# Kernel tuning notes

Hardware: AMD Instinct MI355X
Metric: run time of the kernel (lower is better)

Reference implementation:

```python
import jax, jax.numpy as jnp
import numpy as np


def setup_inputs() -> dict:
    key = jax.random.key(0)
    ks = jax.random.split(key, 5)
    B, C, H, W = 4, 64, 64, 64
    C8 = C // 8
    return {
        "x_opt": jax.random.normal(ks[0], (B, C, H, W), jnp.float32),
        "x_sar": jax.random.normal(ks[1], (B, C, H, W), jnp.float32),
        "wq": jax.random.normal(ks[2], (C8, C), jnp.float32) * 0.05,
        "bq": jnp.zeros((C8,), jnp.float32),
        "wk": jax.random.normal(ks[3], (C8, C), jnp.float32) * 0.05,
        "bk": jnp.zeros((C8,), jnp.float32),
        "wv": jax.random.normal(ks[4], (C, C), jnp.float32) * 0.05,
        "bv": jnp.zeros((C,), jnp.float32),
        "gamma": jnp.zeros((1,), jnp.float32),
    }


def reference(x_opt, x_sar, wq, bq, wk, bk, wv, bv, gamma):
    b, c, h, w = x_opt.shape
    n = h * w
    xo = x_opt.reshape(b, c, n)  # [b, c, N]
    xs = x_sar.reshape(b, c, n)
    # 1x1 convs == channel matmuls
    q = jnp.einsum('oc,bcn->bon', wq, xo) + bq[None, :, None]  # [b, c//8, N]
    k = jnp.einsum('oc,bcn->bon', wk, xs) + bk[None, :, None]  # [b, c//8, N]
    v = jnp.einsum('oc,bcn->bon', wv, xs) + bv[None, :, None]  # [b, c, N]
    # attn[b, n, m] = softmax_m( q[:, :, n] . k[:, :, m] )  -- NO 1/sqrt(d) scaling
    scores = jnp.einsum('bdn,bdm->bnm', q, k)  # [b, N, N]
    attn = jax.nn.softmax(scores, axis=-1)
    # out[b, c, n] = sum_m v[b, c, m] * attn[b, n, m]
    out = jnp.einsum('bcm,bnm->bcn', v, attn).reshape(b, c, h, w)
    return gamma[0] * out + x_opt
```

## Files before the change

### kernel.cpp

```cpp
#include <hip/hip_runtime.h>
#include <hip/hip_bf16.h>
#include <stdint.h>

#define NDIM 4096
#define CDIM 64
#define NSPLIT 8
#define SPAN (NDIM / NSPLIT)
#define KBLK 128
#define NIT (SPAN / KBLK)
#define LOG2E 1.44269504088896f

typedef float f32x16 __attribute__((ext_vector_type(16)));
typedef short bf16x8 __attribute__((ext_vector_type(8)));
union U4B { uint4 u; bf16x8 b; };

static __device__ __forceinline__ uint32_t cvtpk(float lo, float hi) {
  uint32_t r;
  asm("v_cvt_pk_bf16_f32 %0, %1, %2" : "=v"(r) : "v"(lo), "v"(hi));
  return r;
}
static __device__ __forceinline__ uint16_t f2bf(float f) {
  uint32_t r;
  asm("v_cvt_pk_bf16_f32 %0, %1, %1" : "=v"(r) : "v"(f));
  return (uint16_t)r;
}
static __device__ __forceinline__ float fexp2(float x) {
  return __builtin_amdgcn_exp2f(x);
}
static __device__ __forceinline__ void gload_lds16(const void* g, void* l) {
  __builtin_amdgcn_global_load_lds(
      (const __attribute__((address_space(1))) uint32_t*)g,
      (__attribute__((address_space(3))) uint32_t*)l, 16, 0, 0);
}

__global__ __launch_bounds__(256) void proj_kernel(
    const float* __restrict__ x_opt, const float* __restrict__ x_sar,
    const float* __restrict__ wq, const float* __restrict__ bq,
    const float* __restrict__ wk, const float* __restrict__ bk,
    const float* __restrict__ wvp, const float* __restrict__ bv,
    uint16_t* __restrict__ qf, uint16_t* __restrict__ kf,
    uint16_t* __restrict__ vf)
{
  const int tid = threadIdx.x;
  const int w = tid >> 6;
  const int l = tid & 63;
  const int x = l & 31;
  const int hi = l >> 5;
  const int cg = w >> 1;
  const int half = w & 1;

  const int id = blockIdx.x;
  const int b = id >> 6;
  const int n0 = (id & 63) * 64 + cg * 32;
  const size_t xbase = (size_t)b * CDIM * NDIM;

  bf16x8 xsB[4];
#pragma unroll
  for (int kc = 0; kc < 4; kc++) {
    float sv[8];
#pragma unroll
    for (int j = 0; j < 8; j++)
      sv[j] = x_sar[xbase + (size_t)(kc * 16 + hi * 8 + j) * NDIM + n0 + x];
    U4B us;
    us.u = make_uint4(cvtpk(sv[0], sv[1]), cvtpk(sv[2], sv[3]),
                      cvtpk(sv[4], sv[5]), cvtpk(sv[6], sv[7]));
    xsB[kc] = us.b;
  }

  bf16x8 vA[4];
#pragma unroll
  for (int kc = 0; kc < 4; kc++) {
    const float* wr = wvp + (half * 32 + x) * 64 + kc * 16 + hi * 8;
    float4 wa = ((const float4*)wr)[0];
    float4 wb = ((const float4*)wr)[1];
    U4B u;
    u.u = make_uint4(cvtpk(wa.x, wa.y), cvtpk(wa.z, wa.w),
                     cvtpk(wb.x, wb.y), cvtpk(wb.z, wb.w));
    vA[kc] = u.b;
  }

  const f32x16 z16 = {0.f,0.f,0.f,0.f, 0.f,0.f,0.f,0.f,
                      0.f,0.f,0.f,0.f, 0.f,0.f,0.f,0.f};
  f32x16 aV = z16;
#pragma unroll
  for (int kc = 0; kc < 4; kc++)
    aV = __builtin_amdgcn_mfma_f32_32x32x16_bf16(vA[kc], xsB[kc], aV, 0, 0, 0);
#pragma unroll
  for (int r = 0; r < 16; r++) {
    const int row = half * 32 + (r & 3) + 8 * (r >> 2) + 4 * hi;
    vf[(size_t)(b * 64 + row) * NDIM + n0 + x] = f2bf(aV[r] + bv[row]);
  }

  bf16x8 gA[4], gB[4];
#pragma unroll
  for (int kc = 0; kc < 4; kc++) {
    U4B ua;
    ua.u = make_uint4(0u, 0u, 0u, 0u);
    if (x < 8) {
      const float* wr = (half ? wk : wq) + x * 64 + kc * 16 + hi * 8;
      float4 wa = ((const float4*)wr)[0];
      float4 wb = ((const float4*)wr)[1];
      ua.u = make_uint4(cvtpk(wa.x, wa.y), cvtpk(wa.z, wa.w),
                        cvtpk(wb.x, wb.y), cvtpk(wb.z, wb.w));
    }
    gA[kc] = ua.b;
    if (half == 0) {
      float ov[8];
#pragma unroll
      for (int j = 0; j < 8; j++)
        ov[j] = x_opt[xbase + (size_t)(kc * 16 + hi * 8 + j) * NDIM + n0 + x];
      U4B uo;
      uo.u = make_uint4(cvtpk(ov[0], ov[1]), cvtpk(ov[2], ov[3]),
                        cvtpk(ov[4], ov[5]), cvtpk(ov[6], ov[7]));
      gB[kc] = uo.b;
    } else {
      gB[kc] = xsB[kc];
    }
  }
  f32x16 aG = z16;
#pragma unroll
  for (int kc = 0; kc < 4; kc++)
    aG = __builtin_amdgcn_mfma_f32_32x32x16_bf16(gA[kc], gB[kc], aG, 0, 0, 0);

  const float* bias = half ? bk : bq;
  const float scl = half ? 1.0f : LOG2E;
  float gv[4];
#pragma unroll
  for (int r = 0; r < 4; r++) gv[r] = (aG[r] + bias[4 * hi + r]) * scl;
  uint16_t* dst = half ? kf : qf;
  const size_t nrow = ((size_t)b * NDIM + n0 + x) * 16;
  uint2 st;
  st.x = cvtpk(gv[0], gv[1]); st.y = cvtpk(gv[2], gv[3]);
  *(uint2*)(dst + nrow + hi * 4) = st;
  if (hi == 0) {
    const uint4 z4 = make_uint4(0u, 0u, 0u, 0u);
    *(uint4*)(dst + nrow + 8) = z4;
  }
}

__global__ __launch_bounds__(256, 3) void attn_kernel(
    const uint16_t* __restrict__ qf, const uint16_t* __restrict__ kf,
    const uint16_t* __restrict__ vf,
    uint16_t* __restrict__ po, float* __restrict__ ls)
{
  __shared__ __align__(16) uint16_t vt[2][64][128];

  const int tid = threadIdx.x;
  const int w = tid >> 6;
  const int l = tid & 63;
  const int x = l & 31;
  const int hi = l >> 5;

  const int id = blockIdx.x;
  const int sp = id & 7;
  const int qb = (id >> 3) & 31;
  const int b = id >> 8;

  const int n0 = qb * 128;
  const uint16_t* vsrc = vf + (size_t)b * CDIM * NDIM + sp * SPAN;
  const uint16_t* ksrc = kf + ((size_t)b * NDIM + sp * SPAN) * 16;
  const int qrow = n0 + w * 32 + x;

  U4B qfr;
  qfr.u = *(const uint4*)(qf + ((size_t)b * NDIM + qrow) * 16 + hi * 8);

  const uint32_t xh4 = (uint32_t)(((x & 15) ^ hi) << 4);
  const uint8_t* vbase0 = (const uint8_t*)&vt[0][0][0] + (size_t)x * 256 + xh4;
  const uint8_t* vbase1 = vbase0 + 16384;

  const f32x16 z16 = {0.f,0.f,0.f,0.f, 0.f,0.f,0.f,0.f,
                      0.f,0.f,0.f,0.f, 0.f,0.f,0.f,0.f};
  f32x16 oacc0 = z16, oacc1 = z16;
  float lacc[4] = {0.f, 0.f, 0.f, 0.f};

  auto stageV = [&](int t, int buf) {
#pragma unroll
    for (int si = 0; si < 4; si++) {
      const int rowbase = w * 16 + si * 4;
      const int row = rowbase + (l >> 4);
      gload_lds16(vsrc + (size_t)row * NDIM + t * KBLK +
                      (((l & 15) ^ (row & 15)) << 3),
                  &vt[buf][rowbase][0]);
    }
  };

  stageV(0, 0);
  uint4 kc = *(const uint4*)(ksrc + (size_t)x * 16 + hi * 8);
  __syncthreads();
  uint4 kn = *(const uint4*)(ksrc + ((size_t)32 + x) * 16 + hi * 8);
  U4B ka; ka.u = kc;
  f32x16 scur = __builtin_amdgcn_mfma_f32_32x32x16_bf16(ka.b, qfr.b, z16, 0, 0, 0);
  kc = kn;

#pragma unroll
  for (int gq = 0; gq < 16; gq++) {
    const int it = gq >> 2;
    const int q4 = gq & 3;

    if (q4 == 0 && it + 1 < NIT) stageV(it + 1, (it + 1) & 1);

    uint4 kn2 = *(const uint4*)(ksrc + ((size_t)(gq + 2) * 32 + x) * 16 + hi * 8);

    U4B kb; kb.u = kc;
    f32x16 snxt = __builtin_amdgcn_mfma_f32_32x32x16_bf16(kb.b, qfr.b, z16, 0, 0, 0);
    kc = kn2;

    float p[16];
#pragma unroll
    for (int i = 0; i < 16; i++) p[i] = fexp2(scur[i]);
    float t8[8];
#pragma unroll
    for (int i = 0; i < 8; i++) t8[i] = p[i] + p[i + 8];
#pragma unroll
    for (int i = 0; i < 4; i++) lacc[i] += t8[i] + t8[i + 4];

    uint32_t W[8];
#pragma unroll
    for (int j = 0; j < 8; j++) W[j] = cvtpk(p[2 * j], p[2 * j + 1]);

    const uint8_t* vb = (it & 1) ? vbase1 : vbase0;
    __builtin_amdgcn_s_setprio(1);
#pragma unroll
    for (int sub = 0; sub < 2; sub++) {
      uint32_t a0 = W[sub * 4 + 0], b0 = W[sub * 4 + 2];
      uint32_t a1 = W[sub * 4 + 1], b1 = W[sub * 4 + 3];
      asm("v_permlane32_swap_b32 %0, %1" : "+v"(a0), "+v"(b0));
      asm("v_permlane32_swap_b32 %0, %1" : "+v"(a1), "+v"(b1));
      U4B pf;
      pf.u = make_uint4(a0, a1, b0, b1);
      const uint32_t kb4 = (uint32_t)((q4 * 4 + sub * 2) << 4);
      const uint8_t* va = vb + (kb4 ^ xh4) - xh4;
      U4B vf0, vf1;
      vf0.u = *(const uint4*)(va);
      vf1.u = *(const uint4*)(va + 8192);
      oacc0 = __builtin_amdgcn_mfma_f32_32x32x16_bf16(vf0.b, pf.b, oacc0, 0, 0, 0);
      oacc1 = __builtin_amdgcn_mfma_f32_32x32x16_bf16(vf1.b, pf.b, oacc1, 0, 0, 0);
    }
    __builtin_amdgcn_s_setprio(0);

    if (q4 == 3) __syncthreads();
    scur = snxt;
  }

  uint16_t* prow = po + (((size_t)sp * 4 + b) * NDIM + qrow) * CDIM;
#pragma unroll
  for (int cb = 0; cb < 2; cb++) {
    const f32x16 oa = (cb == 0) ? oacc0 : oacc1;
#pragma unroll
    for (int u = 0; u < 4; u++) {
      uint2 st;
      st.x = cvtpk(oa[u * 4 + 0], oa[u * 4 + 1]);
      st.y = cvtpk(oa[u * 4 + 2], oa[u * 4 + 3]);
      *(uint2*)(prow + cb * 32 + u * 8 + hi * 4) = st;
    }
  }
  float ltot = (lacc[0] + lacc[1]) + (lacc[2] + lacc[3]);
  ltot += __shfl_xor(ltot, 32);
  if (hi == 0)
    ls[((size_t)sp * 4 + b) * NDIM + qrow] = ltot;
}

__global__ __launch_bounds__(256) void merge_kernel(
    const uint16_t* __restrict__ po, const float* __restrict__ ls,
    const float* __restrict__ x_opt, const float* __restrict__ gamma,
    float* __restrict__ out)
{
  __shared__ float ot[32][65];
  const int tid = threadIdx.x;
  const int b = blockIdx.x >> 7;
  const int n0 = (blockIdx.x & 127) * 32;
  {
    const int q = tid >> 3;
    const int co = (tid & 7) * 8;
    const int nq = n0 + q;
    float wsum = 0.f;
    float acc[8] = {0.f, 0.f, 0.f, 0.f, 0.f, 0.f, 0.f, 0.f};
#pragma unroll
    for (int s = 0; s < NSPLIT; s++) {
      wsum += ls[((size_t)s * 4 + b) * NDIM + nq];
      const uint4 pv = *(const uint4*)(po + (((size_t)s * 4 + b) * NDIM + nq) * CDIM + co);
      const uint32_t* pw = (const uint32_t*)&pv;
#pragma unroll
      for (int j = 0; j < 4; j++) {
        acc[j * 2 + 0] += __uint_as_float(pw[j] << 16);
        acc[j * 2 + 1] += __uint_as_float(pw[j] & 0xFFFF0000u);
      }
    }
    const float inv = 1.f / wsum;
#pragma unroll
    for (int j = 0; j < 8; j++) ot[q][co + j] = acc[j] * inv;
  }
  __syncthreads();
  {
    const float gm = gamma[0];
    const int c = tid >> 2;
    const int j8 = (tid & 3) * 8;
    const float* xp = x_opt + ((size_t)b * CDIM + c) * NDIM + n0 + j8;
    float* op = out + ((size_t)b * CDIM + c) * NDIM + n0 + j8;
#pragma unroll
    for (int h = 0; h < 2; h++) {
      float4 xv = ((const float4*)xp)[h];
      float4 ov;
      ov.x = gm * ot[j8 + h * 4 + 0][c] + xv.x;
      ov.y = gm * ot[j8 + h * 4 + 1][c] + xv.y;
      ov.z = gm * ot[j8 + h * 4 + 2][c] + xv.z;
      ov.w = gm * ot[j8 + h * 4 + 3][c] + xv.w;
      ((float4*)op)[h] = ov;
    }
  }
}

extern "C" void kernel_launch(void* const* d_in, const int* in_sizes, int n_in,
                              void* d_out, int out_size, void* d_ws, size_t ws_size,
                              hipStream_t stream) {
  const float* x_opt = (const float*)d_in[0];
  const float* x_sar = (const float*)d_in[1];
  const float* wq    = (const float*)d_in[2];
  const float* bq    = (const float*)d_in[3];
  const float* wk    = (const float*)d_in[4];
  const float* bk    = (const float*)d_in[5];
  const float* wvp   = (const float*)d_in[6];
  const float* bv    = (const float*)d_in[7];
  const float* gamma = (const float*)d_in[8];
  float* outp = (float*)d_out;

  uint16_t* qf = (uint16_t*)d_ws;
  uint16_t* kf = (uint16_t*)((char*)d_ws + 524288);
  uint16_t* vf = (uint16_t*)((char*)d_ws + 1048576);
  uint16_t* po = (uint16_t*)((char*)d_ws + 3145728);
  float* lsp   = (float*)((char*)d_ws + 19922944);

  proj_kernel<<<256, 256, 0, stream>>>(x_opt, x_sar, wq, bq, wk, bk, wvp, bv,
                                       qf, kf, vf);
  attn_kernel<<<1024, 256, 0, stream>>>(qf, kf, vf, po, lsp);
  merge_kernel<<<512, 256, 0, stream>>>(po, lsp, x_opt, gamma, outp);
}
```

Baseline: 38.21 us.

## Split projection work across waves and drop score software-pipelining to raise occupancy

The projection kernel now gives each wave one MFMA chain over a 32-column tile: two waves compute V, one Q, one K. The grid doubles to 512 blocks and each wave does a single 4-MFMA sequence instead of two serial ones, which shortens per-wave latency. In the attention kernel, the one-step-ahead score MFMA prefetch is removed and launch_bounds goes from 3 to 4 waves per SIMD, cutting register pressure so more blocks can be resident. This trades explicit MFMA/exp overlap within a wave for more latency hiding across waves, and the x_sar tile is now loaded by three waves in the same block instead of being reused from registers.

```diff
diff --git a/kernel.cpp b/kernel.cpp
--- a/kernel.cpp
+++ b/kernel.cpp
@@ -46,99 +46,79 @@
   const int l = tid & 63;
   const int x = l & 31;
   const int hi = l >> 5;
-  const int cg = w >> 1;
-  const int half = w & 1;
 
   const int id = blockIdx.x;
-  const int b = id >> 6;
-  const int n0 = (id & 63) * 64 + cg * 32;
+  const int b = id >> 7;
+  const int n0 = (id & 127) * 32;
   const size_t xbase = (size_t)b * CDIM * NDIM;
 
-  bf16x8 xsB[4];
+  const float* xsrc = (w == 2) ? x_opt : x_sar;
+  bf16x8 xB[4];
 #pragma unroll
   for (int kc = 0; kc < 4; kc++) {
     float sv[8];
 #pragma unroll
     for (int j = 0; j < 8; j++)
-      sv[j] = x_sar[xbase + (size_t)(kc * 16 + hi * 8 + j) * NDIM + n0 + x];
+      sv[j] = xsrc[xbase + (size_t)(kc * 16 + hi * 8 + j) * NDIM + n0 + x];
     U4B us;
     us.u = make_uint4(cvtpk(sv[0], sv[1]), cvtpk(sv[2], sv[3]),
                       cvtpk(sv[4], sv[5]), cvtpk(sv[6], sv[7]));
-    xsB[kc] = us.b;
-  }
-
-  bf16x8 vA[4];
-#pragma unroll
-  for (int kc = 0; kc < 4; kc++) {
-    const float* wr = wvp + (half * 32 + x) * 64 + kc * 16 + hi * 8;
-    float4 wa = ((const float4*)wr)[0];
-    float4 wb = ((const float4*)wr)[1];
-    U4B u;
-    u.u = make_uint4(cvtpk(wa.x, wa.y), cvtpk(wa.z, wa.w),
-                     cvtpk(wb.x, wb.y), cvtpk(wb.z, wb.w));
-    vA[kc] = u.b;
-  }
-
-  const f32x16 z16 = {0.f,0.f,0.f,0.f, 0.f,0.f,0.f,0.f,
-                      0.f,0.f,0.f,0.f, 0.f,0.f,0.f,0.f};
-  f32x16 aV = z16;
-#pragma unroll
-  for (int kc = 0; kc < 4; kc++)
-    aV = __builtin_amdgcn_mfma_f32_32x32x16_bf16(vA[kc], xsB[kc], aV, 0, 0, 0);
-#pragma unroll
-  for (int r = 0; r < 16; r++) {
-    const int row = half * 32 + (r & 3) + 8 * (r >> 2) + 4 * hi;
-    vf[(size_t)(b * 64 + row) * NDIM + n0 + x] = f2bf(aV[r] + bv[row]);
-  }
-
-  bf16x8 gA[4], gB[4];
+    xB[kc] = us.b;
+  }
+
+  bf16x8 aF[4];
 #pragma unroll
   for (int kc = 0; kc < 4; kc++) {
     U4B ua;
     ua.u = make_uint4(0u, 0u, 0u, 0u);
-    if (x < 8) {
-      const float* wr = (half ? wk : wq) + x * 64 + kc * 16 + hi * 8;
+    if (w < 2) {
+      const float* wr = wvp + (w * 32 + x) * 64 + kc * 16 + hi * 8;
       float4 wa = ((const float4*)wr)[0];
       float4 wb = ((const float4*)wr)[1];
       ua.u = make_uint4(cvtpk(wa.x, wa.y), cvtpk(wa.z, wa.w),
                         cvtpk(wb.x, wb.y), cvtpk(wb.z, wb.w));
-    }
-    gA[kc] = ua.b;
-    if (half == 0) {
-      float ov[8];
-#pragma unroll
-      for (int j = 0; j < 8; j++)
-        ov[j] = x_opt[xbase + (size_t)(kc * 16 + hi * 8 + j) * NDIM + n0 + x];
-      U4B uo;
-      uo.u = make_uint4(cvtpk(ov[0], ov[1]), cvtpk(ov[2], ov[3]),
-                        cvtpk(ov[4], ov[5]), cvtpk(ov[6], ov[7]));
-      gB[kc] = uo.b;
-    } else {
-      gB[kc] = xsB[kc];
-    }
-  }
-  f32x16 aG = z16;
+    } else if (x < 8) {
+      const float* wr = ((w == 2) ? wq : wk) + x * 64 + kc * 16 + hi * 8;
+      float4 wa = ((const float4*)wr)[0];
+      float4 wb = ((const float4*)wr)[1];
+      ua.u = make_uint4(cvtpk(wa.x, wa.y), cvtpk(wa.z, wa.w),
+                        cvtpk(wb.x, wb.y), cvtpk(wb.z, wb.w));
+    }
+    aF[kc] = ua.b;
+  }
+
+  const f32x16 z16 = {0.f,0.f,0.f,0.f, 0.f,0.f,0.f,0.f,
+                      0.f,0.f,0.f,0.f, 0.f,0.f,0.f,0.f};
+  f32x16 acc = z16;
 #pragma unroll
   for (int kc = 0; kc < 4; kc++)
-    aG = __builtin_amdgcn_mfma_f32_32x32x16_bf16(gA[kc], gB[kc], aG, 0, 0, 0);
-
-  const float* bias = half ? bk : bq;
-  const float scl = half ? 1.0f : LOG2E;
-  float gv[4];
-#pragma unroll
-  for (int r = 0; r < 4; r++) gv[r] = (aG[r] + bias[4 * hi + r]) * scl;
-  uint16_t* dst = half ? kf : qf;
-  const size_t nrow = ((size_t)b * NDIM + n0 + x) * 16;
-  uint2 st;
-  st.x = cvtpk(gv[0], gv[1]); st.y = cvtpk(gv[2], gv[3]);
-  *(uint2*)(dst + nrow + hi * 4) = st;
-  if (hi == 0) {
-    const uint4 z4 = make_uint4(0u, 0u, 0u, 0u);
-    *(uint4*)(dst + nrow + 8) = z4;
-  }
-}
-
-__global__ __launch_bounds__(256, 3) void attn_kernel(
+    acc = __builtin_amdgcn_mfma_f32_32x32x16_bf16(aF[kc], xB[kc], acc, 0, 0, 0);
+
+  if (w < 2) {
+#pragma unroll
+    for (int r = 0; r < 16; r++) {
+      const int row = w * 32 + (r & 3) + 8 * (r >> 2) + 4 * hi;
+      vf[(size_t)(b * 64 + row) * NDIM + n0 + x] = f2bf(acc[r] + bv[row]);
+    }
+  } else {
+    const float* bias = (w == 2) ? bq : bk;
+    const float scl = (w == 2) ? LOG2E : 1.0f;
+    float gv[4];
+#pragma unroll
+    for (int r = 0; r < 4; r++) gv[r] = (acc[r] + bias[4 * hi + r]) * scl;
+    uint16_t* dst = (w == 2) ? qf : kf;
+    const size_t nrow = ((size_t)b * NDIM + n0 + x) * 16;
+    uint2 st;
+    st.x = cvtpk(gv[0], gv[1]); st.y = cvtpk(gv[2], gv[3]);
+    *(uint2*)(dst + nrow + hi * 4) = st;
+    if (hi == 0) {
+      const uint4 z4 = make_uint4(0u, 0u, 0u, 0u);
+      *(uint4*)(dst + nrow + 8) = z4;
+    }
+  }
+}
+
+__global__ __launch_bounds__(256, 4) void attn_kernel(
     const uint16_t* __restrict__ qf, const uint16_t* __restrict__ kf,
     const uint16_t* __restrict__ vf,
     uint16_t* __restrict__ po, float* __restrict__ ls)
@@ -165,7 +145,7 @@
   qfr.u = *(const uint4*)(qf + ((size_t)b * NDIM + qrow) * 16 + hi * 8);
 
   const uint32_t xh4 = (uint32_t)(((x & 15) ^ hi) << 4);
-  const uint8_t* vbase0 = (const uint8_t*)&vt[0][0][0] + (size_t)x * 256 + xh4;
+  const uint8_t* vbase0 = (const uint8_t*)&vt[0][0][0] + (size_t)x * 256;
   const uint8_t* vbase1 = vbase0 + 16384;
 
   const f32x16 z16 = {0.f,0.f,0.f,0.f, 0.f,0.f,0.f,0.f,
@@ -187,10 +167,6 @@
   stageV(0, 0);
   uint4 kc = *(const uint4*)(ksrc + (size_t)x * 16 + hi * 8);
   __syncthreads();
-  uint4 kn = *(const uint4*)(ksrc + ((size_t)32 + x) * 16 + hi * 8);
-  U4B ka; ka.u = kc;
-  f32x16 scur = __builtin_amdgcn_mfma_f32_32x32x16_bf16(ka.b, qfr.b, z16, 0, 0, 0);
-  kc = kn;
 
 #pragma unroll
   for (int gq = 0; gq < 16; gq++) {
@@ -199,15 +175,14 @@
 
     if (q4 == 0 && it + 1 < NIT) stageV(it + 1, (it + 1) & 1);
 
-    uint4 kn2 = *(const uint4*)(ksrc + ((size_t)(gq + 2) * 32 + x) * 16 + hi * 8);
-
-    U4B kb; kb.u = kc;
-    f32x16 snxt = __builtin_amdgcn_mfma_f32_32x32x16_bf16(kb.b, qfr.b, z16, 0, 0, 0);
-    kc = kn2;
+    uint4 kn = *(const uint4*)(ksrc + ((size_t)(gq + 1) * 32 + x) * 16 + hi * 8);
+
+    U4B ka; ka.u = kc;
+    f32x16 s = __builtin_amdgcn_mfma_f32_32x32x16_bf16(ka.b, qfr.b, z16, 0, 0, 0);
 
     float p[16];
 #pragma unroll
-    for (int i = 0; i < 16; i++) p[i] = fexp2(scur[i]);
+    for (int i = 0; i < 16; i++) p[i] = fexp2(s[i]);
     float t8[8];
 #pragma unroll
     for (int i = 0; i < 8; i++) t8[i] = p[i] + p[i + 8];
@@ -229,7 +204,7 @@
       U4B pf;
       pf.u = make_uint4(a0, a1, b0, b1);
       const uint32_t kb4 = (uint32_t)((q4 * 4 + sub * 2) << 4);
-      const uint8_t* va = vb + (kb4 ^ xh4) - xh4;
+      const uint8_t* va = vb + (kb4 ^ xh4);
       U4B vf0, vf1;
       vf0.u = *(const uint4*)(va);
       vf1.u = *(const uint4*)(va + 8192);
@@ -239,7 +214,7 @@
     __builtin_amdgcn_s_setprio(0);
 
     if (q4 == 3) __syncthreads();
-    scur = snxt;
+    kc = kn;
   }
 
   uint16_t* prow = po + (((size_t)sp * 4 + b) * NDIM + qrow) * CDIM;
@@ -330,7 +305,7 @@
   uint16_t* po = (uint16_t*)((char*)d_ws + 3145728);
   float* lsp   = (float*)((char*)d_ws + 19922944);
 
-  proj_kernel<<<256, 256, 0, stream>>>(x_opt, x_sar, wq, bq, wk, bk, wvp, bv,
+  proj_kernel<<<512, 256, 0, stream>>>(x_opt, x_sar, wq, bq, wk, bk, wvp, bv,
                                        qf, kf, vf);
   attn_kernel<<<1024, 256, 0, stream>>>(qf, kf, vf, po, lsp);
   merge_kernel<<<512, 256, 0, stream>>>(po, lsp, x_opt, gamma, outp);
```

Result: no change. 38.47 us (+0.7%).
